# Kernel optimization log

Hardware: AMD Instinct MI355X
Metric: run time of the kernel (lower is better)

The kernel has to match this reference:

```python
import jax, jax.numpy as jnp
import numpy as np

W_LEN = 37  # window_length
EPS = 1e-9
LRELU_SLOPE = 0.2
SQRT2 = 1.4142135623730951


def win_sum(x, w):
    # Depthwise sliding-window sum of width w, 'same' padding w//2 (odd w).
    # Equivalent to the diag-kernel conv1d in the original code, but O(T) via cumsum.
    pad = w // 2
    xp = jnp.pad(x, ((0, 0), (0, 0), (pad, pad)))
    cs = jnp.cumsum(xp, axis=-1)
    cs = jnp.pad(cs, ((0, 0), (0, 0), (1, 0)))
    return cs[..., w:] - cs[..., :-w]


def conv1d(x, w, b):
    # x: [B,C,T], w: [O,I,3], padding=1
    y = jax.lax.conv_general_dilated(x, w, (1,), [(1, 1)],
                                     dimension_numbers=('NCH', 'OIH', 'NCH'))
    return y + b[None, :, None]


def adawin_instance(x, s, mask, fc_w, fc_b, alpha):
    # x: [B,C,T], s: [B,S,T], mask: [B,T]
    C = x.shape[1]
    h = jnp.einsum('bst,cs->bct', s, fc_w) + fc_b[None, :, None]  # [B,2C,T]
    m = mask[:, None, :]                       # [B,1,T]
    denom = win_sum(m, W_LEN) + EPS            # same for all channels
    gamma = win_sum(h[:, :C], W_LEN) / denom * m
    beta = win_sum(h[:, C:], W_LEN) / denom * m
    x_norm = jnp.tanh(alpha * x)               # WindowedNorm1d.forward
    return (1.0 + gamma) * x_norm + beta


def setup_inputs() -> dict:
    key = jax.random.key(0)
    ks = jax.random.split(key, 10)
    B, C_IN, C_OUT, S, T = 16, 512, 512, 128, 2048
    inp = {
        'x': jax.random.normal(ks[0], (B, C_IN, T), dtype=jnp.float32),
        's': jax.random.normal(ks[1], (B, S, T), dtype=jnp.float32),
        'lengths': jax.random.randint(ks[2], (B,), 0, T).astype(jnp.int32),
        'fc1_w': jax.random.normal(ks[3], (2 * C_IN, S), dtype=jnp.float32) * 0.05,
        'fc1_b': jnp.zeros((2 * C_IN,), dtype=jnp.float32),
        'alpha1': jnp.full((1,), 0.5, dtype=jnp.float32),
        'conv1_w': jax.random.normal(ks[4], (C_OUT, C_IN, 3), dtype=jnp.float32) * 0.02,
        'conv1_b': jnp.zeros((C_OUT,), dtype=jnp.float32),
        'fc2_w': jax.random.normal(ks[5], (2 * C_OUT, S), dtype=jnp.float32) * 0.05,
        'fc2_b': jnp.zeros((2 * C_OUT,), dtype=jnp.float32),
        'alpha2': jnp.full((1,), 0.5, dtype=jnp.float32),
        'conv2_w': jax.random.normal(ks[6], (C_OUT, C_OUT, 3), dtype=jnp.float32) * 0.02,
        'conv2_b': jnp.zeros((C_OUT,), dtype=jnp.float32),
    }
    return inp


def reference(x, s, lengths, fc1_w, fc1_b, alpha1, conv1_w, conv1_b,
              fc2_w, fc2_b, alpha2, conv2_w, conv2_b):
    T = x.shape[2]
    mask = (jnp.arange(T)[None, :] < lengths[:, None]).astype(x.dtype)  # [B,T]

    h = adawin_instance(x, s, mask, fc1_w, fc1_b, alpha1)
    h = jax.nn.leaky_relu(h, LRELU_SLOPE)
    h = conv1d(h, conv1_w, conv1_b)
    h = adawin_instance(h, s, mask, fc2_w, fc2_b, alpha2)
    h = jax.nn.leaky_relu(h, LRELU_SLOPE)
    h = conv1d(h, conv2_w, conv2_b)

    # dim_in == dim_out -> identity shortcut
    return (h + x) / SQRT2
```

## Files before the change

### kernel.cpp

```cpp
#include <hip/hip_runtime.h>

#define B_ 16
#define C_ 512
#define S_ 128
#define T_ 2048
#define HALF 18
#define WLEN 37

typedef __bf16 bf16x8 __attribute__((ext_vector_type(8)));
typedef float f32x4 __attribute__((ext_vector_type(4)));
typedef float f32x16 __attribute__((ext_vector_type(16)));
typedef unsigned short ushort_t;

__device__ inline ushort_t f2bf(float x) {
    unsigned u = __float_as_uint(x);
    u += 0x7fffu + ((u >> 16) & 1u);
    return (ushort_t)(u >> 16);
}
__device__ inline float bf2f(ushort_t h) {
    return __uint_as_float(((unsigned)h) << 16);
}
__device__ inline float fast_tanh(float z) {
    float e = __expf(2.f * z);
    return 1.f - __fdividef(2.f, e + 1.f);
}
__device__ __forceinline__ void glds16(const void* g, void* l) {
    __builtin_amdgcn_global_load_lds(
        (const __attribute__((address_space(1))) unsigned*)g,
        (__attribute__((address_space(3))) unsigned*)l, 16, 0, 0);
}

#define MFMA16(a, b, c) __builtin_amdgcn_mfma_f32_16x16x32_bf16((a), (b), (c), 0, 0, 0)
#define MFMA32(a, b, c) __builtin_amdgcn_mfma_f32_32x32x16_bf16((a), (b), (c), 0, 0, 0)

#define ACH_BYTES 28672
#define BCH_BYTES 13312
#define CH_BYTES (ACH_BYTES + BCH_BYTES)

__global__ __launch_bounds__(256) void prep_all(
    const float* __restrict__ s, ushort_t* __restrict__ sw_t,
    const float* __restrict__ fc1, const float* __restrict__ fc2,
    ushort_t* __restrict__ Wfc, const float* __restrict__ c1,
    const float* __restrict__ c2, ushort_t* __restrict__ I1,
    ushort_t* __restrict__ I2, ushort_t* __restrict__ y1p,
    ushort_t* __restrict__ y2p) {
    __shared__ float sb[128][101];
    int bid = blockIdx.x;
    int tid = threadIdx.x;
    if (bid < 512) {
        int b = bid >> 5;
        int t0 = (bid & 31) * 64;
        for (int e = tid; e < 128 * 100; e += 256) {
            int sj = e / 100;
            int u = e - sj * 100;
            int gt = t0 - HALF + u;
            float v = 0.f;
            if (gt >= 0 && gt < T_) v = s[((size_t)(b * S_ + sj)) * T_ + gt];
            sb[sj][u] = v;
        }
        __syncthreads();
        for (int e = tid; e < 64 * 128; e += 256) {
            int tl = e >> 7;
            int sj = e & 127;
            float sum = 0.f;
#pragma unroll
            for (int d = 0; d < WLEN; ++d) sum += sb[sj][tl + d];
            sw_t[((size_t)(b * T_ + t0 + tl)) * S_ + sj] = f2bf(sum);
        }
    } else if (bid < 1408) {
        int idx = (bid - 512) * 256 + tid;
        const int per_conv = 2 * 32 * 1792;
        int conv = idx >= per_conv;
        int rr = conv ? idx - per_conv : idx;
        const float* src = conv ? c2 : c1;
        ushort_t* dst = conv ? I2 : I1;
        int chunk_id = rr / 1792;
        int srem = rr - chunk_id * 1792;
        int mb = chunk_id >> 5, cc = chunk_id & 31;
        int off = srem * 16;
        int row = off / 112;
        int c = off - row * 112;
        ushort_t vals[8];
        if (c >= 96) {
#pragma unroll
            for (int e = 0; e < 8; ++e) vals[e] = 0;
        } else {
            int tap = c >> 5;
            int ch_lo = (c & 31) >> 1;
            int o = mb * 256 + row;
            int ibase = cc * 16 + ch_lo;
#pragma unroll
            for (int e = 0; e < 8; ++e)
                vals[e] = f2bf(src[(size_t)(o * 512 + ibase + e) * 3 + tap]);
        }
        uint4 pk;
        pk.x = vals[0] | ((unsigned)vals[1] << 16);
        pk.y = vals[2] | ((unsigned)vals[3] << 16);
        pk.z = vals[4] | ((unsigned)vals[5] << 16);
        pk.w = vals[6] | ((unsigned)vals[7] << 16);
        *(uint4*)&dst[(size_t)rr * 8] = pk;
    } else if (bid < 2432) {
        const int n_fc = 1024 * 128;
        int idx = (bid - 1408) * 256 + tid;
        if (idx < n_fc) Wfc[idx] = f2bf(fc1[idx]);
        else if (idx < 2 * n_fc) Wfc[idx] = f2bf(fc2[idx - n_fc]);
    } else {
        int t2 = (bid - 2432) * 256 + tid;
        if (t2 < 4096) {
            ushort_t* base = (t2 & 1) ? y2p : y1p;
            int r = t2 >> 1;
            int bb = r >> 7;
            int rowsel = (r >> 6) & 1;
            int col = (r & 63) * 8;
            size_t row = (size_t)bb * (T_ + 2) + (rowsel ? (T_ + 1) : 0);
            *(uint4*)&base[row * C_ + col] = (uint4){0, 0, 0, 0};
        }
    }
}

template <int INLAYOUT>
__global__ __launch_bounds__(256) void adawin_kernel(
    const void* __restrict__ xin_, const ushort_t* __restrict__ sw_t,
    const ushort_t* __restrict__ Wfc, const float* __restrict__ fcb,
    const float* __restrict__ alpha, const int* __restrict__ lengths,
    ushort_t* __restrict__ youtp) {
    int t0 = blockIdx.x * 64;
    int c0 = blockIdx.y * 64;
    int b = blockIdx.z;
    __shared__ __attribute__((aligned(16))) ushort_t smem[128 * 136 + 64 * 136];
    ushort_t (*As)[136] = (ushort_t(*)[136])smem;
    ushort_t (*Bs)[136] = (ushort_t(*)[136])(smem + 128 * 136);
    int tid = threadIdx.x;

    {
        int r = tid >> 4;
        int cseg = (tid & 15) * 8;
#pragma unroll
        for (int p = 0; p < 8; ++p) {
            int row = p * 16 + r;
            int grow = (row < 64) ? (c0 + row) : (448 + c0 + row);
            *(uint4*)&As[row][cseg] = *(const uint4*)&Wfc[(size_t)grow * 128 + cseg];
        }
    }
    {
        int tl = tid & 63;
        int sg = tid >> 6;
        const ushort_t* src = &sw_t[((size_t)(b * T_ + t0 + tl)) * S_];
#pragma unroll
        for (int j = 0; j < 4; ++j) {
            int col = sg * 32 + j * 8;
            *(uint4*)&Bs[tl][col] = *(const uint4*)&src[col];
        }
    }
    __syncthreads();

    int wave = tid >> 6, lane = tid & 63;
    int quad = lane >> 4, l = lane & 15;
    f32x4 accg[4], accb[4];
#pragma unroll
    for (int n = 0; n < 4; ++n) {
        accg[n] = (f32x4){0.f, 0.f, 0.f, 0.f};
        accb[n] = (f32x4){0.f, 0.f, 0.f, 0.f};
    }
    int rg = wave * 16 + l;
    int rb = 64 + wave * 16 + l;
#pragma unroll
    for (int ks = 0; ks < 4; ++ks) {
        int kc = ks * 32 + quad * 8;
        bf16x8 ag = *(const bf16x8*)&As[rg][kc];
        bf16x8 ab = *(const bf16x8*)&As[rb][kc];
#pragma unroll
        for (int n = 0; n < 4; ++n) {
            bf16x8 bb = *(const bf16x8*)&Bs[n * 16 + l][kc];
            accg[n] = MFMA16(ag, bb, accg[n]);
            accb[n] = MFMA16(ab, bb, accb[n]);
        }
    }

    __syncthreads();
    ushort_t (*Ts)[72] = (ushort_t(*)[72])smem;

    int len = lengths[b];
    float alph = alpha[0];
    const float* xf = (const float*)xin_;
    const ushort_t* xh = (const ushort_t*)xin_;
    int clocal = wave * 16 + quad * 4;
    int cbase = c0 + clocal;
#pragma unroll
    for (int n = 0; n < 4; ++n) {
        int t = t0 + n * 16 + l;
        int lo = t - HALF; if (lo < 0) lo = 0;
        int hi = t + HALF; if (hi > T_ - 1) hi = T_ - 1;
        float cnt = (float)(hi - lo + 1);
        int hv = hi < (len - 1) ? hi : (len - 1);
        int mdi = hv - lo + 1; if (mdi < 0) mdi = 0;
        float m = (t < len) ? 1.f : 0.f;
        float sc = m / ((float)mdi + 1e-9f);

        float xv[4];
        if (INLAYOUT == 0) {
#pragma unroll
            for (int j = 0; j < 4; ++j)
                xv[j] = xf[(size_t)(b * C_ + cbase + j) * T_ + t];
        } else {
            uint2 xraw = *(const uint2*)&xh[((size_t)(b * (T_ + 2) + 1 + t)) * C_ + cbase];
            xv[0] = bf2f((ushort_t)(xraw.x & 0xffff));
            xv[1] = bf2f((ushort_t)(xraw.x >> 16));
            xv[2] = bf2f((ushort_t)(xraw.y & 0xffff));
            xv[3] = bf2f((ushort_t)(xraw.y >> 16));
        }
        unsigned pk[2];
#pragma unroll
        for (int j = 0; j < 4; ++j) {
            int c = cbase + j;
            float gamma = (accg[n][j] + fcb[c] * cnt) * sc;
            float beta = (accb[n][j] + fcb[C_ + c] * cnt) * sc;
            float xn = fast_tanh(alph * xv[j]);
            float v = (1.f + gamma) * xn + beta;
            v = v > 0.f ? v : 0.2f * v;
            unsigned hv16 = (unsigned)f2bf(v);
            if (j & 1) pk[j >> 1] |= hv16 << 16;
            else pk[j >> 1] = hv16;
        }
        *(uint2*)&Ts[n * 16 + l][clocal] = (uint2){pk[0], pk[1]};
    }
    __syncthreads();
    {
        int row = tid >> 2;
        int seg = (tid & 3) * 16;
        size_t gbase = ((size_t)(b * (T_ + 2) + 1 + t0 + row)) * C_ + c0 + seg;
        *(uint4*)&youtp[gbase] = *(const uint4*)&Ts[row][seg];
        *(uint4*)&youtp[gbase + 8] = *(const uint4*)&Ts[row][seg + 8];
    }
}

__device__ __forceinline__ void stage_chunk(const char* img, const char* xt, int cc,
                                            char* buf, int wave, int lane) {
    char* Ab = buf;
    char* Bb = buf + ACH_BYTES;
#pragma unroll
    for (int k = 0; k < 6; ++k) {
        int g = wave + 8 * k;
        if (g < 28) {
            glds16(img + g * 1024 + lane * 16, Ab + g * 1024);
        } else if (g < 41) {
            int j = g - 28;
            int off = j * 1024 + lane * 16;
            int r = off / 48;
            int sl = (off - r * 48) >> 4;
            if (sl == 2) sl = 0;
            if (r > 257) r = 257;
            glds16(xt + (size_t)r * 1024 + cc * 32 + sl * 16, Bb + j * 1024);
        } else {
            int j = g - 41;
            glds16(img + j * 1024 + lane * 16, Ab + j * 1024);
        }
    }
}

template <int EPI>
__global__ __launch_bounds__(512, 2) void conv_kernel(
    const ushort_t* __restrict__ Xp, const ushort_t* __restrict__ Wimg,
    const float* __restrict__ bias, const float* __restrict__ resid,
    ushort_t* __restrict__ out_bf, float* __restrict__ out_f) {
    int t0 = blockIdx.x * 256;
    int o0 = blockIdx.y * 256;
    int b = blockIdx.z;
    __shared__ __attribute__((aligned(16))) char smem[135168];
    int tid = threadIdx.x;
    int lane = tid & 63, wave = tid >> 6;
    int l32 = lane & 31, khalf = lane >> 5;
    int wm = wave >> 2, wn = wave & 3;

    const char* imgcc = (const char*)Wimg + (size_t)blockIdx.y * 32 * ACH_BYTES;
    const char* xt = (const char*)Xp + (size_t)(b * (T_ + 2) + t0) * 1024;

    f32x16 acc[4][2];
#pragma unroll
    for (int m = 0; m < 4; ++m)
#pragma unroll
        for (int nf = 0; nf < 2; ++nf)
#pragma unroll
            for (int r = 0; r < 16; ++r) acc[m][nf][r] = 0.f;

    stage_chunk(imgcc, xt, 0, smem, wave, lane);
    stage_chunk(imgcc + ACH_BYTES, xt, 1, smem + CH_BYTES, wave, lane);
    asm volatile("s_waitcnt vmcnt(6)" ::: "memory");
    asm volatile("s_barrier" ::: "memory");

    int cur = 0;
#pragma unroll 1
    for (int c = 0; c < 32; ++c) {
        char* buf = smem + cur * CH_BYTES;
        if (c + 2 < 32) {
            int s2 = cur + 2; if (s2 >= 3) s2 -= 3;
            stage_chunk(imgcc + (size_t)(c + 2) * ACH_BYTES, xt, c + 2,
                        smem + s2 * CH_BYTES, wave, lane);
        }
        ushort_t (*As)[56] = (ushort_t(*)[56])buf;
        ushort_t (*Bs)[24] = (ushort_t(*)[24])(buf + ACH_BYTES);
#pragma unroll
        for (int p = 0; p < 3; ++p) {
            bf16x8 a[4], bv[2];
#pragma unroll
            for (int m = 0; m < 4; ++m)
                a[m] = *(const bf16x8*)&As[wm * 128 + m * 32 + l32][p * 16 + khalf * 8];
#pragma unroll
            for (int nf = 0; nf < 2; ++nf)
                bv[nf] = *(const bf16x8*)&Bs[wn * 64 + nf * 32 + l32 + p][khalf * 8];
#pragma unroll
            for (int m = 0; m < 4; ++m)
#pragma unroll
                for (int nf = 0; nf < 2; ++nf)
                    acc[m][nf] = MFMA32(a[m], bv[nf], acc[m][nf]);
        }
        if (c + 2 < 32) asm volatile("s_waitcnt vmcnt(6)" ::: "memory");
        else if (c + 1 < 32) asm volatile("s_waitcnt vmcnt(0)" ::: "memory");
        asm volatile("s_barrier" ::: "memory");
        cur = cur + 1; if (cur >= 3) cur = 0;
    }

    if (EPI == 0) {
        __syncthreads();
        ushort_t (*Ts)[264] = (ushort_t(*)[264])smem;
#pragma unroll
        for (int nf = 0; nf < 2; ++nf) {
            int trow = wn * 64 + nf * 32 + l32;
#pragma unroll
            for (int m = 0; m < 4; ++m) {
#pragma unroll
                for (int g = 0; g < 4; ++g) {
                    int oc = wm * 128 + m * 32 + g * 8 + khalf * 4;
                    unsigned pk[2];
#pragma unroll
                    for (int j = 0; j < 4; ++j) {
                        float v = acc[m][nf][g * 4 + j] + bias[o0 + oc + j];
                        unsigned hv16 = (unsigned)f2bf(v);
                        if (j & 1) pk[j >> 1] |= hv16 << 16;
                        else pk[j >> 1] = hv16;
                    }
                    *(uint2*)&Ts[trow][oc] = (uint2){pk[0], pk[1]};
                }
            }
        }
        __syncthreads();
        int row = tid >> 1;
        int colh = (tid & 1) * 128;
        size_t gbase = ((size_t)(b * (T_ + 2) + 1 + t0 + row)) * C_ + o0 + colh;
#pragma unroll
        for (int j = 0; j < 16; ++j)
            *(uint4*)&out_bf[gbase + j * 8] = *(const uint4*)&Ts[row][colh + j * 8];
    } else {
#pragma unroll
        for (int m = 0; m < 4; ++m)
#pragma unroll
            for (int nf = 0; nf < 2; ++nf) {
                int t = t0 + wn * 64 + nf * 32 + l32;
#pragma unroll
                for (int g = 0; g < 4; ++g) {
                    int oo = o0 + wm * 128 + m * 32 + g * 8 + khalf * 4;
#pragma unroll
                    for (int j = 0; j < 4; ++j) {
                        size_t off = (size_t)(b * C_ + oo + j) * T_ + t;
                        out_f[off] = (acc[m][nf][g * 4 + j] + bias[oo + j] + resid[off]) *
                                     0.70710678118654752f;
                    }
                }
            }
    }
}

extern "C" void kernel_launch(void* const* d_in, const int* in_sizes, int n_in,
                              void* d_out, int out_size, void* d_ws, size_t ws_size,
                              hipStream_t stream) {
    const float* x = (const float*)d_in[0];
    const float* s = (const float*)d_in[1];
    const int* lengths = (const int*)d_in[2];
    const float* fc1_w = (const float*)d_in[3];
    const float* fc1_b = (const float*)d_in[4];
    const float* alpha1 = (const float*)d_in[5];
    const float* conv1_w = (const float*)d_in[6];
    const float* conv1_b = (const float*)d_in[7];
    const float* fc2_w = (const float*)d_in[8];
    const float* fc2_b = (const float*)d_in[9];
    const float* alpha2 = (const float*)d_in[10];
    const float* conv2_w = (const float*)d_in[11];
    const float* conv2_b = (const float*)d_in[12];

    const size_t IMGB = (size_t)2 * 32 * ACH_BYTES;
    char* ws = (char*)d_ws;
    ushort_t* sw_t = (ushort_t*)ws; ws += (size_t)B_ * T_ * S_ * 2;
    ushort_t* Wfc = (ushort_t*)ws;  ws += (size_t)2 * 1024 * 128 * 2;
    ushort_t* I1 = (ushort_t*)ws;   ws += IMGB;
    ushort_t* I2 = (ushort_t*)ws;   ws += IMGB;
    ushort_t* y2p = (ushort_t*)ws;  ws += (size_t)B_ * (T_ + 2) * C_ * 2;
    ushort_t* y1p = (ushort_t*)ws;  ws += (size_t)B_ * (T_ + 2) * C_ * 2;
    ws += 12 * 1024;
    if ((size_t)(ws - (char*)d_ws) > ws_size) return;

    prep_all<<<dim3(2448), dim3(256), 0, stream>>>(
        s, sw_t, fc1_w, fc2_w, Wfc, conv1_w, conv2_w, I1, I2, y1p, y2p);
    adawin_kernel<0><<<dim3(32, 8, 16), dim3(256), 0, stream>>>(
        (const void*)x, sw_t, Wfc, fc1_b, alpha1, lengths, y1p);
    conv_kernel<0><<<dim3(8, 2, 16), dim3(512), 0, stream>>>(
        y1p, I1, conv1_b, (const float*)nullptr, y2p, (float*)nullptr);
    adawin_kernel<1><<<dim3(32, 8, 16), dim3(256), 0, stream>>>(
        (const void*)y2p, sw_t, Wfc + 1024 * 128, fc2_b, alpha2, lengths, y1p);
    conv_kernel<1><<<dim3(8, 2, 16), dim3(512), 0, stream>>>(
        y1p, I2, conv2_b, x, (ushort_t*)nullptr, (float*)d_out);
}
```

Measured before the change: 347.1 us.

## Shrink conv tiles to 128x128 with double-buffered staging and more resident blocks

The conv kernel drops from 256x256 output tiles with 8 waves and a 3-stage LDS ring to 128x128 tiles with 4 waves and a 2-stage buffer. The smaller LDS footprint and 256-thread blocks (launch bounds 256,3) are meant to fit more blocks per CU, and the grid grows from 256 to 1024 blocks. The weight image layout in prep is rebuilt for 128-row output blocks. In exchange each block does less MFMA work per staged byte and now waits on the current chunk right after issuing the prefetch, so there is less overlap between loads and math.

```diff
diff --git a/kernel.cpp b/kernel.cpp
--- a/kernel.cpp
+++ b/kernel.cpp
@@ -33,8 +33,8 @@
 #define MFMA16(a, b, c) __builtin_amdgcn_mfma_f32_16x16x32_bf16((a), (b), (c), 0, 0, 0)
 #define MFMA32(a, b, c) __builtin_amdgcn_mfma_f32_32x32x16_bf16((a), (b), (c), 0, 0, 0)
 
-#define ACH_BYTES 28672
-#define BCH_BYTES 13312
+#define ACH_BYTES 14336
+#define BCH_BYTES 7168
 #define CH_BYTES (ACH_BYTES + BCH_BYTES)
 
 __global__ __launch_bounds__(256) void prep_all(
@@ -69,14 +69,14 @@
         }
     } else if (bid < 1408) {
         int idx = (bid - 512) * 256 + tid;
-        const int per_conv = 2 * 32 * 1792;
+        const int per_conv = 4 * 32 * 896;
         int conv = idx >= per_conv;
         int rr = conv ? idx - per_conv : idx;
         const float* src = conv ? c2 : c1;
         ushort_t* dst = conv ? I2 : I1;
-        int chunk_id = rr / 1792;
-        int srem = rr - chunk_id * 1792;
-        int mb = chunk_id >> 5, cc = chunk_id & 31;
+        int chunk_id = rr / 896;
+        int srem = rr - chunk_id * 896;
+        int ob = chunk_id >> 5, cc = chunk_id & 31;
         int off = srem * 16;
         int row = off / 112;
         int c = off - row * 112;
@@ -86,9 +86,9 @@
             for (int e = 0; e < 8; ++e) vals[e] = 0;
         } else {
             int tap = c >> 5;
-            int ch_lo = (c & 31) >> 1;
-            int o = mb * 256 + row;
-            int ibase = cc * 16 + ch_lo;
+            int kh8 = (c & 16) ? 8 : 0;
+            int o = ob * 128 + row;
+            int ibase = cc * 16 + kh8;
 #pragma unroll
             for (int e = 0; e < 8; ++e)
                 vals[e] = f2bf(src[(size_t)(o * 512 + ibase + e) * 3 + tap]);
@@ -235,106 +235,95 @@
 }
 
 __device__ __forceinline__ void stage_chunk(const char* img, const char* xt, int cc,
-                                            char* buf, int wave, int lane) {
-    char* Ab = buf;
-    char* Bb = buf + ACH_BYTES;
+                                            char* Ab, char* Bb, int wave, int lane) {
 #pragma unroll
     for (int k = 0; k < 6; ++k) {
-        int g = wave + 8 * k;
-        if (g < 28) {
+        int g = wave + 4 * k;
+        if (g >= 21) continue;
+        if (g < 14) {
             glds16(img + g * 1024 + lane * 16, Ab + g * 1024);
-        } else if (g < 41) {
-            int j = g - 28;
+        } else {
+            int j = g - 14;
             int off = j * 1024 + lane * 16;
             int r = off / 48;
             int sl = (off - r * 48) >> 4;
             if (sl == 2) sl = 0;
-            if (r > 257) r = 257;
+            if (r > 129) r = 129;
             glds16(xt + (size_t)r * 1024 + cc * 32 + sl * 16, Bb + j * 1024);
-        } else {
-            int j = g - 41;
-            glds16(img + j * 1024 + lane * 16, Ab + j * 1024);
         }
     }
 }
 
 template <int EPI>
-__global__ __launch_bounds__(512, 2) void conv_kernel(
+__global__ __launch_bounds__(256, 3) void conv_kernel(
     const ushort_t* __restrict__ Xp, const ushort_t* __restrict__ Wimg,
     const float* __restrict__ bias, const float* __restrict__ resid,
     ushort_t* __restrict__ out_bf, float* __restrict__ out_f) {
-    int t0 = blockIdx.x * 256;
-    int o0 = blockIdx.y * 256;
+    int t0 = blockIdx.x * 128;
+    int o0 = blockIdx.y * 128;
     int b = blockIdx.z;
-    __shared__ __attribute__((aligned(16))) char smem[135168];
+    __shared__ __attribute__((aligned(16))) char smem[2 * CH_BYTES];
     int tid = threadIdx.x;
     int lane = tid & 63, wave = tid >> 6;
     int l32 = lane & 31, khalf = lane >> 5;
-    int wm = wave >> 2, wn = wave & 3;
-
-    const char* imgcc = (const char*)Wimg + (size_t)blockIdx.y * 32 * ACH_BYTES;
+    int wo = (wave & 1) * 64, wt = (wave >> 1) * 64;
+
+    const char* imgbase = (const char*)Wimg + (size_t)blockIdx.y * 32 * ACH_BYTES;
     const char* xt = (const char*)Xp + (size_t)(b * (T_ + 2) + t0) * 1024;
 
-    f32x16 acc[4][2];
-#pragma unroll
-    for (int m = 0; m < 4; ++m)
-#pragma unroll
-        for (int nf = 0; nf < 2; ++nf)
-#pragma unroll
-            for (int r = 0; r < 16; ++r) acc[m][nf][r] = 0.f;
-
-    stage_chunk(imgcc, xt, 0, smem, wave, lane);
-    stage_chunk(imgcc + ACH_BYTES, xt, 1, smem + CH_BYTES, wave, lane);
-    asm volatile("s_waitcnt vmcnt(6)" ::: "memory");
-    asm volatile("s_barrier" ::: "memory");
-
-    int cur = 0;
+    f32x16 acc[2][2];
+#pragma unroll
+    for (int io = 0; io < 2; ++io)
+#pragma unroll
+        for (int it = 0; it < 2; ++it)
+#pragma unroll
+            for (int r = 0; r < 16; ++r) acc[io][it][r] = 0.f;
+
+    stage_chunk(imgbase, xt, 0, smem, smem + ACH_BYTES, wave, lane);
+
 #pragma unroll 1
     for (int c = 0; c < 32; ++c) {
-        char* buf = smem + cur * CH_BYTES;
-        if (c + 2 < 32) {
-            int s2 = cur + 2; if (s2 >= 3) s2 -= 3;
-            stage_chunk(imgcc + (size_t)(c + 2) * ACH_BYTES, xt, c + 2,
-                        smem + s2 * CH_BYTES, wave, lane);
-        }
-        ushort_t (*As)[56] = (ushort_t(*)[56])buf;
-        ushort_t (*Bs)[24] = (ushort_t(*)[24])(buf + ACH_BYTES);
+        int cur = c & 1;
+        char* Ab = smem + cur * CH_BYTES;
+        if (c < 31) {
+            char* An = smem + (cur ^ 1) * CH_BYTES;
+            stage_chunk(imgbase + (size_t)(c + 1) * ACH_BYTES, xt, c + 1,
+                        An, An + ACH_BYTES, wave, lane);
+            if (wave == 0) asm volatile("s_waitcnt vmcnt(6)\ns_barrier" ::: "memory");
+            else           asm volatile("s_waitcnt vmcnt(5)\ns_barrier" ::: "memory");
+        } else {
+            asm volatile("s_waitcnt vmcnt(0)\ns_barrier" ::: "memory");
+        }
+        ushort_t (*As)[56] = (ushort_t(*)[56])Ab;
+        ushort_t (*Bs)[24] = (ushort_t(*)[24])(Ab + ACH_BYTES);
 #pragma unroll
         for (int p = 0; p < 3; ++p) {
-            bf16x8 a[4], bv[2];
-#pragma unroll
-            for (int m = 0; m < 4; ++m)
-                a[m] = *(const bf16x8*)&As[wm * 128 + m * 32 + l32][p * 16 + khalf * 8];
-#pragma unroll
-            for (int nf = 0; nf < 2; ++nf)
-                bv[nf] = *(const bf16x8*)&Bs[wn * 64 + nf * 32 + l32 + p][khalf * 8];
-#pragma unroll
-            for (int m = 0; m < 4; ++m)
-#pragma unroll
-                for (int nf = 0; nf < 2; ++nf)
-                    acc[m][nf] = MFMA32(a[m], bv[nf], acc[m][nf]);
-        }
-        if (c + 2 < 32) asm volatile("s_waitcnt vmcnt(6)" ::: "memory");
-        else if (c + 1 < 32) asm volatile("s_waitcnt vmcnt(0)" ::: "memory");
+            bf16x8 a0 = *(const bf16x8*)&As[wo + l32][p * 16 + khalf * 8];
+            bf16x8 a1 = *(const bf16x8*)&As[wo + 32 + l32][p * 16 + khalf * 8];
+            bf16x8 b0 = *(const bf16x8*)&Bs[wt + l32 + p][khalf * 8];
+            bf16x8 b1 = *(const bf16x8*)&Bs[wt + 32 + l32 + p][khalf * 8];
+            acc[0][0] = MFMA32(a0, b0, acc[0][0]);
+            acc[0][1] = MFMA32(a0, b1, acc[0][1]);
+            acc[1][0] = MFMA32(a1, b0, acc[1][0]);
+            acc[1][1] = MFMA32(a1, b1, acc[1][1]);
+        }
         asm volatile("s_barrier" ::: "memory");
-        cur = cur + 1; if (cur >= 3) cur = 0;
     }
 
     if (EPI == 0) {
-        __syncthreads();
-        ushort_t (*Ts)[264] = (ushort_t(*)[264])smem;
-#pragma unroll
-        for (int nf = 0; nf < 2; ++nf) {
-            int trow = wn * 64 + nf * 32 + l32;
-#pragma unroll
-            for (int m = 0; m < 4; ++m) {
+        ushort_t (*Ts)[136] = (ushort_t(*)[136])smem;
+#pragma unroll
+        for (int io = 0; io < 2; ++io)
+#pragma unroll
+            for (int it = 0; it < 2; ++it) {
+                int trow = wt + it * 32 + l32;
 #pragma unroll
                 for (int g = 0; g < 4; ++g) {
-                    int oc = wm * 128 + m * 32 + g * 8 + khalf * 4;
+                    int oc = wo + io * 32 + g * 8 + khalf * 4;
                     unsigned pk[2];
 #pragma unroll
                     for (int j = 0; j < 4; ++j) {
-                        float v = acc[m][nf][g * 4 + j] + bias[o0 + oc + j];
+                        float v = acc[io][it][g * 4 + j] + bias[o0 + oc + j];
                         unsigned hv16 = (unsigned)f2bf(v);
                         if (j & 1) pk[j >> 1] |= hv16 << 16;
                         else pk[j >> 1] = hv16;
@@ -342,27 +331,29 @@
                     *(uint2*)&Ts[trow][oc] = (uint2){pk[0], pk[1]};
                 }
             }
-        }
         __syncthreads();
-        int row = tid >> 1;
-        int colh = (tid & 1) * 128;
-        size_t gbase = ((size_t)(b * (T_ + 2) + 1 + t0 + row)) * C_ + o0 + colh;
-#pragma unroll
-        for (int j = 0; j < 16; ++j)
-            *(uint4*)&out_bf[gbase + j * 8] = *(const uint4*)&Ts[row][colh + j * 8];
+        int cc = (tid & 15) * 8;
+        int rbse = tid >> 4;
+#pragma unroll
+        for (int j = 0; j < 8; ++j) {
+            int row = j * 16 + rbse;
+            *(uint4*)&out_bf[((size_t)(b * (T_ + 2) + 1 + t0 + row)) * C_ + o0 + cc] =
+                *(const uint4*)&Ts[row][cc];
+        }
     } else {
 #pragma unroll
-        for (int m = 0; m < 4; ++m)
-#pragma unroll
-            for (int nf = 0; nf < 2; ++nf) {
-                int t = t0 + wn * 64 + nf * 32 + l32;
+        for (int io = 0; io < 2; ++io)
+#pragma unroll
+            for (int it = 0; it < 2; ++it) {
+                int obase = o0 + wo + io * 32;
+                int t = t0 + wt + it * 32 + l32;
 #pragma unroll
                 for (int g = 0; g < 4; ++g) {
-                    int oo = o0 + wm * 128 + m * 32 + g * 8 + khalf * 4;
+                    int oo = obase + g * 8 + khalf * 4;
 #pragma unroll
                     for (int j = 0; j < 4; ++j) {
                         size_t off = (size_t)(b * C_ + oo + j) * T_ + t;
-                        out_f[off] = (acc[m][nf][g * 4 + j] + bias[oo + j] + resid[off]) *
+                        out_f[off] = (acc[io][it][g * 4 + j] + bias[oo + j] + resid[off]) *
                                      0.70710678118654752f;
                     }
                 }
@@ -387,7 +378,7 @@
     const float* conv2_w = (const float*)d_in[11];
     const float* conv2_b = (const float*)d_in[12];
 
-    const size_t IMGB = (size_t)2 * 32 * ACH_BYTES;
+    const size_t IMGB = (size_t)4 * 32 * ACH_BYTES;
     char* ws = (char*)d_ws;
     ushort_t* sw_t = (ushort_t*)ws; ws += (size_t)B_ * T_ * S_ * 2;
     ushort_t* Wfc = (ushort_t*)ws;  ws += (size_t)2 * 1024 * 128 * 2;
@@ -402,10 +393,10 @@
         s, sw_t, fc1_w, fc2_w, Wfc, conv1_w, conv2_w, I1, I2, y1p, y2p);
     adawin_kernel<0><<<dim3(32, 8, 16), dim3(256), 0, stream>>>(
         (const void*)x, sw_t, Wfc, fc1_b, alpha1, lengths, y1p);
-    conv_kernel<0><<<dim3(8, 2, 16), dim3(512), 0, stream>>>(
+    conv_kernel<0><<<dim3(16, 4, 16), dim3(256), 0, stream>>>(
         y1p, I1, conv1_b, (const float*)nullptr, y2p, (float*)nullptr);
     adawin_kernel<1><<<dim3(32, 8, 16), dim3(256), 0, stream>>>(
         (const void*)y2p, sw_t, Wfc + 1024 * 128, fc2_b, alpha2, lengths, y1p);
-    conv_kernel<1><<<dim3(8, 2, 16), dim3(512), 0, stream>>>(
+    conv_kernel<1><<<dim3(16, 4, 16), dim3(256), 0, stream>>>(
         y1p, I2, conv2_b, x, (ushort_t*)nullptr, (float*)d_out);
 }
```

After: 354.5 us. 2.1% more time.
